# Performance work log

Measured on AMD Instinct MI355X. Metric: run time of the kernel, lower is better.

Reference implementation:

```python
import jax, jax.numpy as jnp
import numpy as np

N, P, E, HID = 20000, 12, 640000, 100

def setup_inputs() -> dict:
    key = jax.random.key(0)
    ks = jax.random.split(key, 20)
    inp = {}
    inp['x'] = jax.random.normal(ks[0], (N, P), dtype=jnp.float32)
    inp['edge_index'] = jax.random.randint(ks[1], (2, E), 0, N, dtype=jnp.int64)
    inp['edge_weight'] = jax.random.uniform(ks[2], (E,), dtype=jnp.float32)
    s = 0.1
    # GCNConv weights (in=1, out=HID) and biases for z, r, h gates
    inp['W_z'] = jax.random.normal(ks[3], (1, HID)) * s
    inp['b_z'] = jnp.zeros((HID,))
    inp['W_r'] = jax.random.normal(ks[4], (1, HID)) * s
    inp['b_r'] = jnp.zeros((HID,))
    inp['W_h'] = jax.random.normal(ks[5], (1, HID)) * s
    inp['b_h'] = jnp.zeros((HID,))
    # TGCN linear layers: Linear(2*HID, HID), stored as (in, out)
    inp['Wl_z'] = jax.random.normal(ks[6], (2 * HID, HID)) * s
    inp['bl_z'] = jnp.zeros((HID,))
    inp['Wl_r'] = jax.random.normal(ks[7], (2 * HID, HID)) * s
    inp['bl_r'] = jnp.zeros((HID,))
    inp['Wl_h'] = jax.random.normal(ks[8], (2 * HID, HID)) * s
    inp['bl_h'] = jnp.zeros((HID,))
    # A3TGCN temporal attention logits over periods
    inp['att'] = jax.random.uniform(ks[9], (P,))
    # final Linear(100, 1)
    inp['W_out'] = jax.random.normal(ks[10], (HID, 1)) * s
    inp['b_out'] = jnp.zeros((1,))
    return inp

def _gcn_aggregate(x_np, edge_index, edge_weight):
    # symmetric GCN normalization with self-loops (PyG gcn_norm), then
    # aggregate neighbor features: out[i] = sum_j norm_ij * x[j]
    n = x_np.shape[0]
    src, dst = edge_index[0], edge_index[1]
    loop = jnp.arange(n)
    s = jnp.concatenate([src, loop])
    d = jnp.concatenate([dst, loop])
    w = jnp.concatenate([edge_weight, jnp.ones((n,), dtype=x_np.dtype)])
    deg = jax.ops.segment_sum(w, d, num_segments=n)
    dinv = jnp.where(deg > 0, deg ** -0.5, 0.0)
    norm = dinv[s] * w * dinv[d]                      # (E+N,)
    msgs = norm[:, None] * x_np[s]                    # (E+N, P)
    return jax.ops.segment_sum(msgs, d, num_segments=n)  # (N, P)

def reference(x, edge_index, edge_weight, W_z, b_z, W_r, b_r, W_h, b_h,
              Wl_z, bl_z, Wl_r, bl_r, Wl_h, bl_h, att, W_out, b_out):
    # x: (N, P) -> viewed as (N, in_channels=1, P) in the torch module.
    # GCNConv is linear in x, so aggregate once and apply each gate's weight.
    agg = _gcn_aggregate(x, edge_index, edge_weight)       # (N, P)
    C_z = agg[:, :, None] * W_z[0] + b_z                   # (N, P, HID)
    C_r = agg[:, :, None] * W_r[0] + b_r
    C_h = agg[:, :, None] * W_h[0] + b_h
    # A3TGCN calls TGCN with H=None (zeros) for every period independently.
    H0 = jnp.zeros_like(C_z)
    Z = jax.nn.sigmoid(jnp.concatenate([C_z, H0], -1) @ Wl_z + bl_z)
    R = jax.nn.sigmoid(jnp.concatenate([C_r, H0], -1) @ Wl_r + bl_r)
    Ht = jnp.tanh(jnp.concatenate([C_h, H0 * R], -1) @ Wl_h + bl_h)
    Hp = Z * H0 + (1.0 - Z) * Ht                           # (N, P, HID)
    probs = jax.nn.softmax(att)                            # (P,)
    H_acc = jnp.einsum('npo,p->no', Hp, probs)             # (N, HID)
    h = jax.nn.relu(H_acc)
    return h @ W_out + b_out                               # (N, 1)
```

## Files before the change

kernel.cpp:

```cpp
#include <hip/hip_runtime.h>
#include <hip/hip_bf16.h>

constexpr int N_NODES = 20000;
constexpr int P_PER   = 12;
constexpr int N_EDGES = 640000;
constexpr int HID     = 100;

constexpr int BIN_W   = 64;
constexpr int NB      = (N_NODES + BIN_W - 1) / BIN_W;
constexpr int BCAP    = 2560;
constexpr int NBLK2   = 320;
constexpr int CHUNK   = N_EDGES / NBLK2;
constexpr int CUR_STR = 16;
constexpr int Y_STR   = 16;

constexpr size_t OFF_DINV  = 0;
constexpr size_t OFF_UZ    = OFF_DINV + N_NODES;
constexpr size_t OFF_CZ    = OFF_UZ + HID;
constexpr size_t OFF_UH    = OFF_CZ + HID;
constexpr size_t OFF_CH    = OFF_UH + HID;
constexpr size_t OFF_PROBS = OFF_CH + HID;
constexpr size_t OFF_CUR   = 20416;
constexpr size_t OFF_Y     = OFF_CUR + (size_t)NB * CUR_STR;
constexpr size_t OFF_SEG   = OFF_Y + (size_t)N_NODES * Y_STR;
constexpr size_t OFF_SEG2  = OFF_SEG + (size_t)NB * BCAP * 2;
constexpr size_t OFF_ROW   = OFF_SEG2 + (size_t)NB * BCAP * 2;

__global__ void precompute_kernel(const float* __restrict__ Wz, const float* __restrict__ bz,
                                  const float* __restrict__ Wh, const float* __restrict__ bh,
                                  const float* __restrict__ Wlz, const float* __restrict__ blz,
                                  const float* __restrict__ Wlh, const float* __restrict__ blh,
                                  const float* __restrict__ att,
                                  float* __restrict__ uz, float* __restrict__ cz,
                                  float* __restrict__ uh, float* __restrict__ ch,
                                  float* __restrict__ probs) {
    int t = threadIdx.x;
    if (t < HID) {
        float suz = 0.f, scz = 0.f, suh = 0.f, sch = 0.f;
        for (int j = 0; j < HID; ++j) {
            float wlz = Wlz[j * HID + t];
            float wlh = Wlh[j * HID + t];
            suz += Wz[j] * wlz;
            scz += bz[j] * wlz;
            suh += Wh[j] * wlh;
            sch += bh[j] * wlh;
        }
        uz[t] = suz;
        cz[t] = scz + blz[t];
        uh[t] = suh;
        ch[t] = sch + blh[t];
    }
    if (t == 0) {
        float m = att[0];
        for (int p = 1; p < P_PER; ++p) m = fmaxf(m, att[p]);
        float e[P_PER];
        float s = 0.f;
        for (int p = 0; p < P_PER; ++p) { e[p] = __expf(att[p] - m); s += e[p]; }
        float inv = 1.0f / s;
        for (int p = 0; p < P_PER; ++p) probs[p] = e[p] * inv;
    }
}

__global__ __launch_bounds__(256) void partition_kernel(const int* __restrict__ ei,
                                                        const float* __restrict__ w,
                                                        int* __restrict__ cur,
                                                        int2* __restrict__ seg) {
    __shared__ int hist[NB];
    __shared__ int base[NB];
    __shared__ int run[NB];
    int t = threadIdx.x;
    for (int b = t; b < NB; b += 256) { hist[b] = 0; run[b] = 0; }
    __syncthreads();
    int e0 = blockIdx.x * CHUNK;
    const int* __restrict__ dsts = ei + N_EDGES;
    for (int i = t; i < CHUNK; i += 256) {
        int d = dsts[e0 + i];
        atomicAdd(&hist[d >> 6], 1);
    }
    __syncthreads();
    for (int b = t; b < NB; b += 256) {
        int h = hist[b];
        base[b] = (h > 0) ? atomicAdd(cur + (size_t)b * CUR_STR, h) : 0;
    }
    __syncthreads();
    for (int i = t; i < CHUNK; i += 256) {
        int s = ei[e0 + i];
        int d = dsts[e0 + i];
        float wt = w[e0 + i];
        int b = d >> 6;
        int pos = base[b] + atomicAdd(&run[b], 1);
        if (pos < BCAP)
            seg[(size_t)b * BCAP + pos] = make_int2(s | ((d & 63) << 16), __float_as_int(wt));
    }
}

__global__ __launch_bounds__(256) void binsort_kernel(const int2* __restrict__ seg,
                                                      const int* __restrict__ cur,
                                                      const float* __restrict__ x,
                                                      float* __restrict__ dinv,
                                                      float* __restrict__ y,
                                                      int2* __restrict__ seg2,
                                                      int2* __restrict__ rowinfo) {
    __shared__ int2 ent[BCAP];
    __shared__ int2 ent2[BCAP];
    __shared__ int  hist[BIN_W];
    __shared__ int  off[BIN_W];
    __shared__ int  excl[BIN_W];
    __shared__ float sdinv[BIN_W];
    int t = threadIdx.x;
    int b = blockIdx.x;
    if (t < BIN_W) hist[t] = 0;
    __syncthreads();
    int c = min(cur[(size_t)b * CUR_STR], BCAP);
    const int2* sg = seg + (size_t)b * BCAP;
    for (int i = t; i < c; i += 256) {
        int2 e = sg[i];
        ent[i] = e;
        atomicAdd(&hist[e.x >> 16], 1);
    }
    __syncthreads();
    if (t < 64) {
        int v = hist[t];
        int inc = v;
#pragma unroll
        for (int o = 1; o < 64; o <<= 1) {
            int u = __shfl_up(inc, o, 64);
            if (t >= o) inc += u;
        }
        int ex = inc - v;
        excl[t] = ex;
        off[t]  = ex;
    }
    __syncthreads();
    for (int i = t; i < c; i += 256) {
        int2 e = ent[i];
        int dl = e.x >> 16;
        int p = atomicAdd(&off[dl], 1);
        ent2[p] = make_int2(e.x & 0xFFFF, e.y);
    }
    __syncthreads();
    {
        int nl = t >> 2, l = t & 3;
        int beg = excl[nl];
        int end = beg + hist[nl];
        float s = 0.f;
        for (int j = beg + l; j < end; j += 4) s += __int_as_float(ent2[j].y);
        s += __shfl_xor(s, 1, 64);
        s += __shfl_xor(s, 2, 64);
        if (l == 0) sdinv[nl] = rsqrtf(1.0f + s);
    }
    __syncthreads();
    int n0 = b * BIN_W;
    int2* s2 = seg2 + (size_t)b * BCAP;
    for (int i = t; i < c; i += 256) s2[i] = ent2[i];
    if (t < BIN_W && n0 + t < N_NODES) {
        dinv[n0 + t] = sdinv[t];
        rowinfo[n0 + t] = make_int2(b * BCAP + excl[t], hist[t]);
    }
    for (int i = t; i < BIN_W * P_PER; i += 256) {
        int nl = i / P_PER, p = i - nl * P_PER;
        int n = n0 + nl;
        if (n < N_NODES) y[(size_t)n * Y_STR + p] = sdinv[nl] * x[(size_t)n * P_PER + p];
    }
}

__global__ __launch_bounds__(256) void gather_finalize_kernel(const int2* __restrict__ seg2,
                                                              const int2* __restrict__ rowinfo,
                                                              const float* __restrict__ y,
                                                              const float* __restrict__ dinv,
                                                              const float* __restrict__ uz,
                                                              const float* __restrict__ cz,
                                                              const float* __restrict__ uh,
                                                              const float* __restrict__ ch,
                                                              const float* __restrict__ probs,
                                                              const float* __restrict__ Wout,
                                                              const float* __restrict__ bout,
                                                              float* __restrict__ out) {
    __shared__ float s_uz[HID], s_cz[HID], s_uh[HID], s_ch[HID], s_wo[HID];
    __shared__ float s_pr[P_PER];
    int t = threadIdx.x;
    if (t < HID) {
        s_uz[t] = uz[t]; s_cz[t] = cz[t];
        s_uh[t] = uh[t]; s_ch[t] = ch[t];
        s_wo[t] = Wout[t];
    }
    if (t < P_PER) s_pr[t] = probs[t];
    __syncthreads();

    int tid = blockIdx.x * blockDim.x + t;
    int n = tid >> 4;
    int l = tid & 15;
    if (n >= N_NODES) return;

    int2 ri = rowinfo[n];
    float acc[P_PER];
#pragma unroll
    for (int p = 0; p < P_PER; ++p) acc[p] = 0.f;
    int end = ri.x + ri.y;
    for (int j = ri.x + l; j < end; j += 16) {
        int2 e = seg2[j];
        float wt = __int_as_float(e.y);
        const float4* yr = (const float4*)(y + (size_t)e.x * Y_STR);
        float4 y0 = yr[0], y1 = yr[1], y2 = yr[2];
        acc[0]  += wt * y0.x;  acc[1]  += wt * y0.y;
        acc[2]  += wt * y0.z;  acc[3]  += wt * y0.w;
        acc[4]  += wt * y1.x;  acc[5]  += wt * y1.y;
        acc[6]  += wt * y1.z;  acc[7]  += wt * y1.w;
        acc[8]  += wt * y2.x;  acc[9]  += wt * y2.y;
        acc[10] += wt * y2.z;  acc[11] += wt * y2.w;
    }
#pragma unroll
    for (int off = 8; off >= 1; off >>= 1) {
#pragma unroll
        for (int p = 0; p < P_PER; ++p) acc[p] += __shfl_xor(acc[p], off, 64);
    }
    {
        float dn = dinv[n];
        const float4* yr = (const float4*)(y + (size_t)n * Y_STR);
        float4 y0 = yr[0], y1 = yr[1], y2 = yr[2];
        acc[0]  = dn * (acc[0]  + y0.x);  acc[1]  = dn * (acc[1]  + y0.y);
        acc[2]  = dn * (acc[2]  + y0.z);  acc[3]  = dn * (acc[3]  + y0.w);
        acc[4]  = dn * (acc[4]  + y1.x);  acc[5]  = dn * (acc[5]  + y1.y);
        acc[6]  = dn * (acc[6]  + y1.z);  acc[7]  = dn * (acc[7]  + y1.w);
        acc[8]  = dn * (acc[8]  + y2.x);  acc[9]  = dn * (acc[9]  + y2.y);
        acc[10] = dn * (acc[10] + y2.z);  acc[11] = dn * (acc[11] + y2.w);
    }
    float rk = 0.f;
    for (int k = l; k < HID; k += 16) {
        float uzk = s_uz[k], czk = s_cz[k], uhk = s_uh[k], chk = s_ch[k];
        float a2 = 0.f;
#pragma unroll
        for (int p = 0; p < P_PER; ++p) {
            float av = acc[p];
            float vz = fminf(fmaxf(av * uzk + czk, -30.f), 30.f);
            float vh = fminf(fmaxf(av * uhk + chk, -15.f), 15.f);
            float ez  = __expf(vz);
            float e2h = __expf(2.0f * vh);
            float term = (e2h - 1.0f) / ((1.0f + ez) * (e2h + 1.0f));
            a2 += s_pr[p] * term;
        }
        rk += fmaxf(a2, 0.0f) * s_wo[k];
    }
#pragma unroll
    for (int off = 8; off >= 1; off >>= 1) rk += __shfl_xor(rk, off, 64);
    if (l == 0) out[n] = rk + bout[0];
}

extern "C" void kernel_launch(void* const* d_in, const int* in_sizes, int n_in,
                              void* d_out, int out_size, void* d_ws, size_t ws_size,
                              hipStream_t stream) {
    const float* x   = (const float*)d_in[0];
    const int*   ei  = (const int*)d_in[1];
    const float* ew  = (const float*)d_in[2];
    const float* Wz  = (const float*)d_in[3];
    const float* bz  = (const float*)d_in[4];
    const float* Wh  = (const float*)d_in[7];
    const float* bh  = (const float*)d_in[8];
    const float* Wlz = (const float*)d_in[9];
    const float* blz = (const float*)d_in[10];
    const float* Wlh = (const float*)d_in[13];
    const float* blh = (const float*)d_in[14];
    const float* att = (const float*)d_in[15];
    const float* Wout = (const float*)d_in[16];
    const float* bout = (const float*)d_in[17];
    float* out = (float*)d_out;

    float* ws      = (float*)d_ws;
    float* dinv    = ws + OFF_DINV;
    float* uz      = ws + OFF_UZ;
    float* cz      = ws + OFF_CZ;
    float* uh      = ws + OFF_UH;
    float* ch      = ws + OFF_CH;
    float* probs   = ws + OFF_PROBS;
    int*   cur     = (int*)(ws + OFF_CUR);
    float* y       = ws + OFF_Y;
    int2*  seg     = (int2*)(ws + OFF_SEG);
    int2*  seg2    = (int2*)(ws + OFF_SEG2);
    int2*  rowinfo = (int2*)(ws + OFF_ROW);

    hipMemsetAsync(cur, 0, (size_t)NB * CUR_STR * sizeof(int), stream);
    hipLaunchKernelGGL(precompute_kernel, dim3(1), dim3(128), 0, stream,
                       Wz, bz, Wh, bh, Wlz, blz, Wlh, blh, att, uz, cz, uh, ch, probs);
    hipLaunchKernelGGL(partition_kernel, dim3(NBLK2), dim3(256), 0, stream,
                       ei, ew, cur, seg);
    hipLaunchKernelGGL(binsort_kernel, dim3(NB), dim3(256), 0, stream,
                       seg, cur, x, dinv, y, seg2, rowinfo);
    hipLaunchKernelGGL(gather_finalize_kernel, dim3((N_NODES * 16 + 255) / 256), dim3(256), 0, stream,
                       seg2, rowinfo, y, dinv, uz, cz, uh, ch, probs, Wout, bout, out);
}
```

Baseline: 157.3 us.

## Fold memset into precompute, pack dinv into rowinfo, use 8 lanes per node

The separate memset of the bin counters is replaced by zeroing inside the precompute kernel, which saves one launch. The binsort kernel drops its first shared staging buffer and reads segment entries from global memory twice. This halves its LDS use and may allow more resident blocks. dinv is packed into an int4 rowinfo record, so the gather kernel skips a separate load. The gather/finalize kernel now uses 8 lanes per node instead of 16, which means fewer shuffle reduction steps but more serial edge and hidden-unit work per lane.

```diff
diff --git a/kernel.cpp b/kernel.cpp
--- a/kernel.cpp
+++ b/kernel.cpp
@@ -13,6 +13,7 @@
 constexpr int CHUNK   = N_EDGES / NBLK2;
 constexpr int CUR_STR = 16;
 constexpr int Y_STR   = 16;
+constexpr int GL      = 8;
 
 constexpr size_t OFF_DINV  = 0;
 constexpr size_t OFF_UZ    = OFF_DINV + N_NODES;
@@ -26,15 +27,17 @@
 constexpr size_t OFF_SEG2  = OFF_SEG + (size_t)NB * BCAP * 2;
 constexpr size_t OFF_ROW   = OFF_SEG2 + (size_t)NB * BCAP * 2;
 
-__global__ void precompute_kernel(const float* __restrict__ Wz, const float* __restrict__ bz,
-                                  const float* __restrict__ Wh, const float* __restrict__ bh,
-                                  const float* __restrict__ Wlz, const float* __restrict__ blz,
-                                  const float* __restrict__ Wlh, const float* __restrict__ blh,
-                                  const float* __restrict__ att,
-                                  float* __restrict__ uz, float* __restrict__ cz,
-                                  float* __restrict__ uh, float* __restrict__ ch,
-                                  float* __restrict__ probs) {
-    int t = threadIdx.x;
+__global__ __launch_bounds__(256) void precompute_kernel(
+        const float* __restrict__ Wz, const float* __restrict__ bz,
+        const float* __restrict__ Wh, const float* __restrict__ bh,
+        const float* __restrict__ Wlz, const float* __restrict__ blz,
+        const float* __restrict__ Wlh, const float* __restrict__ blh,
+        const float* __restrict__ att,
+        float* __restrict__ uz, float* __restrict__ cz,
+        float* __restrict__ uh, float* __restrict__ ch,
+        float* __restrict__ probs, int* __restrict__ cur) {
+    int t = threadIdx.x;
+    for (int i = t; i < NB * CUR_STR; i += 256) cur[i] = 0;
     if (t < HID) {
         float suz = 0.f, scz = 0.f, suh = 0.f, sch = 0.f;
         for (int j = 0; j < HID; ++j) {
@@ -97,11 +100,9 @@
 __global__ __launch_bounds__(256) void binsort_kernel(const int2* __restrict__ seg,
                                                       const int* __restrict__ cur,
                                                       const float* __restrict__ x,
-                                                      float* __restrict__ dinv,
                                                       float* __restrict__ y,
                                                       int2* __restrict__ seg2,
-                                                      int2* __restrict__ rowinfo) {
-    __shared__ int2 ent[BCAP];
+                                                      int4* __restrict__ rowinfo) {
     __shared__ int2 ent2[BCAP];
     __shared__ int  hist[BIN_W];
     __shared__ int  off[BIN_W];
@@ -113,11 +114,7 @@
     __syncthreads();
     int c = min(cur[(size_t)b * CUR_STR], BCAP);
     const int2* sg = seg + (size_t)b * BCAP;
-    for (int i = t; i < c; i += 256) {
-        int2 e = sg[i];
-        ent[i] = e;
-        atomicAdd(&hist[e.x >> 16], 1);
-    }
+    for (int i = t; i < c; i += 256) atomicAdd(&hist[sg[i].x >> 16], 1);
     __syncthreads();
     if (t < 64) {
         int v = hist[t];
@@ -133,7 +130,7 @@
     }
     __syncthreads();
     for (int i = t; i < c; i += 256) {
-        int2 e = ent[i];
+        int2 e = sg[i];
         int dl = e.x >> 16;
         int p = atomicAdd(&off[dl], 1);
         ent2[p] = make_int2(e.x & 0xFFFF, e.y);
@@ -153,10 +150,9 @@
     int n0 = b * BIN_W;
     int2* s2 = seg2 + (size_t)b * BCAP;
     for (int i = t; i < c; i += 256) s2[i] = ent2[i];
-    if (t < BIN_W && n0 + t < N_NODES) {
-        dinv[n0 + t] = sdinv[t];
-        rowinfo[n0 + t] = make_int2(b * BCAP + excl[t], hist[t]);
-    }
+    if (t < BIN_W && n0 + t < N_NODES)
+        rowinfo[n0 + t] = make_int4(b * BCAP + excl[t], hist[t],
+                                    __float_as_int(sdinv[t]), 0);
     for (int i = t; i < BIN_W * P_PER; i += 256) {
         int nl = i / P_PER, p = i - nl * P_PER;
         int n = n0 + nl;
@@ -165,9 +161,8 @@
 }
 
 __global__ __launch_bounds__(256) void gather_finalize_kernel(const int2* __restrict__ seg2,
-                                                              const int2* __restrict__ rowinfo,
+                                                              const int4* __restrict__ rowinfo,
                                                               const float* __restrict__ y,
-                                                              const float* __restrict__ dinv,
                                                               const float* __restrict__ uz,
                                                               const float* __restrict__ cz,
                                                               const float* __restrict__ uh,
@@ -188,16 +183,16 @@
     __syncthreads();
 
     int tid = blockIdx.x * blockDim.x + t;
-    int n = tid >> 4;
-    int l = tid & 15;
+    int n = tid >> 3;
+    int l = tid & (GL - 1);
     if (n >= N_NODES) return;
 
-    int2 ri = rowinfo[n];
+    int4 ri = rowinfo[n];
     float acc[P_PER];
 #pragma unroll
     for (int p = 0; p < P_PER; ++p) acc[p] = 0.f;
     int end = ri.x + ri.y;
-    for (int j = ri.x + l; j < end; j += 16) {
+    for (int j = ri.x + l; j < end; j += GL) {
         int2 e = seg2[j];
         float wt = __int_as_float(e.y);
         const float4* yr = (const float4*)(y + (size_t)e.x * Y_STR);
@@ -210,12 +205,12 @@
         acc[10] += wt * y2.z;  acc[11] += wt * y2.w;
     }
 #pragma unroll
-    for (int off = 8; off >= 1; off >>= 1) {
+    for (int off = 4; off >= 1; off >>= 1) {
 #pragma unroll
         for (int p = 0; p < P_PER; ++p) acc[p] += __shfl_xor(acc[p], off, 64);
     }
     {
-        float dn = dinv[n];
+        float dn = __int_as_float(ri.z);
         const float4* yr = (const float4*)(y + (size_t)n * Y_STR);
         float4 y0 = yr[0], y1 = yr[1], y2 = yr[2];
         acc[0]  = dn * (acc[0]  + y0.x);  acc[1]  = dn * (acc[1]  + y0.y);
@@ -226,7 +221,7 @@
         acc[10] = dn * (acc[10] + y2.z);  acc[11] = dn * (acc[11] + y2.w);
     }
     float rk = 0.f;
-    for (int k = l; k < HID; k += 16) {
+    for (int k = l; k < HID; k += GL) {
         float uzk = s_uz[k], czk = s_cz[k], uhk = s_uh[k], chk = s_ch[k];
         float a2 = 0.f;
 #pragma unroll
@@ -242,7 +237,7 @@
         rk += fmaxf(a2, 0.0f) * s_wo[k];
     }
 #pragma unroll
-    for (int off = 8; off >= 1; off >>= 1) rk += __shfl_xor(rk, off, 64);
+    for (int off = 4; off >= 1; off >>= 1) rk += __shfl_xor(rk, off, 64);
     if (l == 0) out[n] = rk + bout[0];
 }
 
@@ -266,7 +261,6 @@
     float* out = (float*)d_out;
 
     float* ws      = (float*)d_ws;
-    float* dinv    = ws + OFF_DINV;
     float* uz      = ws + OFF_UZ;
     float* cz      = ws + OFF_CZ;
     float* uh      = ws + OFF_UH;
@@ -276,15 +270,14 @@
     float* y       = ws + OFF_Y;
     int2*  seg     = (int2*)(ws + OFF_SEG);
     int2*  seg2    = (int2*)(ws + OFF_SEG2);
-    int2*  rowinfo = (int2*)(ws + OFF_ROW);
-
-    hipMemsetAsync(cur, 0, (size_t)NB * CUR_STR * sizeof(int), stream);
-    hipLaunchKernelGGL(precompute_kernel, dim3(1), dim3(128), 0, stream,
-                       Wz, bz, Wh, bh, Wlz, blz, Wlh, blh, att, uz, cz, uh, ch, probs);
+    int4*  rowinfo = (int4*)(ws + OFF_ROW);
+
+    hipLaunchKernelGGL(precompute_kernel, dim3(1), dim3(256), 0, stream,
+                       Wz, bz, Wh, bh, Wlz, blz, Wlh, blh, att, uz, cz, uh, ch, probs, cur);
     hipLaunchKernelGGL(partition_kernel, dim3(NBLK2), dim3(256), 0, stream,
                        ei, ew, cur, seg);
     hipLaunchKernelGGL(binsort_kernel, dim3(NB), dim3(256), 0, stream,
-                       seg, cur, x, dinv, y, seg2, rowinfo);
-    hipLaunchKernelGGL(gather_finalize_kernel, dim3((N_NODES * 16 + 255) / 256), dim3(256), 0, stream,
-                       seg2, rowinfo, y, dinv, uz, cz, uh, ch, probs, Wout, bout, out);
-}
+                       seg, cur, x, y, seg2, rowinfo);
+    hipLaunchKernelGGL(gather_finalize_kernel, dim3((N_NODES * GL + 255) / 256), dim3(256), 0, stream,
+                       seg2, rowinfo, y, uz, cz, uh, ch, probs, Wout, bout, out);
+}
```

Measured after the change: 157.4 us. Within noise of the previous version (+0.1%).
